# Optimization experiments

Measured on AMD Instinct MI355X. Metric: run time of the kernel, lower is better.

Reference implementation:

```python
import jax, jax.numpy as jnp
import numpy as np

D_MODEL = 1024
NUM_HEADS = 16


def setup_inputs() -> dict:
    key = jax.random.key(0)
    ks = jax.random.split(key, 11)
    B, T, D = 4, 2048, D_MODEL
    scale = 1.0 / np.sqrt(D)
    inp = {
        'q': jax.random.normal(ks[0], (B, T, D), jnp.float32),
        'k': jax.random.normal(ks[1], (B, T, D), jnp.float32),
        'v': jax.random.normal(ks[2], (B, T, D), jnp.float32),
        'W_q': jax.random.normal(ks[3], (D, D), jnp.float32) * scale,
        'b_q': jnp.zeros((D,), jnp.float32),
        'W_k': jax.random.normal(ks[4], (D, D), jnp.float32) * scale,
        'b_k': jnp.zeros((D,), jnp.float32),
        'W_v': jax.random.normal(ks[5], (D, D), jnp.float32) * scale,
        'b_v': jnp.zeros((D,), jnp.float32),
        'W_o': jax.random.normal(ks[6], (D, D), jnp.float32) * scale,
        'b_o': jnp.zeros((D,), jnp.float32),
    }
    return inp


def reference(q, k, v, W_q, b_q, W_k, b_k, W_v, b_v, W_o, b_o):
    B, T, D = q.shape
    H = NUM_HEADS
    hd = D // H  # head dim

    def split_heads(x):  # [B,T,D] -> [B,H,T,hd]
        return x.reshape(B, T, H, hd).transpose(0, 2, 1, 3)

    qh = split_heads(q @ W_q + b_q)
    kh = split_heads(k @ W_k + b_k)
    vh = split_heads(v @ W_v + b_v)

    score = jnp.einsum('bhqd,bhkd->bhqk', qh, kh) / jnp.sqrt(jnp.float32(hd))
    attn = jax.nn.softmax(score, axis=-1)
    out = jnp.einsum('bhqk,bhkd->bhqd', attn, vh)  # [B,H,T,hd]
    out = out.transpose(0, 2, 1, 3).reshape(B, T, D)
    return out @ W_o + b_o
```

## Files before the change

kernel.cpp:

```cpp
#include <hip/hip_runtime.h>

typedef __attribute__((ext_vector_type(8))) short s8v;
typedef __attribute__((ext_vector_type(4))) float f4v;
typedef __attribute__((ext_vector_type(16))) float f16v;
typedef __attribute__((ext_vector_type(8))) unsigned short u8v;
typedef __attribute__((ext_vector_type(4))) unsigned short u16x4;
typedef __attribute__((ext_vector_type(4))) unsigned int uint4v;

#define B_ 4
#define T_ 2048
#define D_ 1024
#define H_ 16
#define HD_ 64

__device__ __forceinline__ unsigned short f2bf(float f) {
  unsigned int u = __builtin_bit_cast(unsigned int, f);
  u += 0x7fffu + ((u >> 16) & 1u);
  return (unsigned short)(u >> 16);
}

__device__ __forceinline__ unsigned int packbf2(float lo, float hi) {
  unsigned int u0 = __builtin_bit_cast(unsigned int, lo) + 0x8000u;
  unsigned int u1 = __builtin_bit_cast(unsigned int, hi) + 0x8000u;
  return __builtin_amdgcn_perm(u1, u0, 0x07060302u);
}

__device__ __forceinline__ void gload_lds16(const void* g, void* l) {
  __builtin_amdgcn_global_load_lds(
      (const __attribute__((address_space(1))) unsigned int*)g,
      (__attribute__((address_space(3))) unsigned int*)l, 16, 0, 0);
}

__global__ __launch_bounds__(256) void cvt_bf16(const float* __restrict__ x,
                                                unsigned short* __restrict__ y) {
  size_t i = ((size_t)blockIdx.x * 256 + threadIdx.x) * 8;
  float4 a = *(const float4*)(x + i);
  float4 b = *(const float4*)(x + i + 4);
  u8v o;
  o[0] = f2bf(a.x); o[1] = f2bf(a.y); o[2] = f2bf(a.z); o[3] = f2bf(a.w);
  o[4] = f2bf(b.x); o[5] = f2bf(b.y); o[6] = f2bf(b.z); o[7] = f2bf(b.w);
  *(u8v*)(y + i) = o;
}

__global__ __launch_bounds__(256) void wt_cvt(
    const float* __restrict__ Wq, const float* __restrict__ Wk,
    const float* __restrict__ Wv, const float* __restrict__ Wo,
    unsigned short* __restrict__ Tq, unsigned short* __restrict__ Tk,
    unsigned short* __restrict__ Tv, unsigned short* __restrict__ To) {
  __shared__ unsigned short tile[32][33];
  int z = blockIdx.z;
  const float* W = (z == 0) ? Wq : (z == 1) ? Wk : (z == 2) ? Wv : Wo;
  unsigned short* Wt = (z == 0) ? Tq : (z == 1) ? Tk : (z == 2) ? Tv : To;
  int k0 = blockIdx.x * 32, n0 = blockIdx.y * 32;
  int t = threadIdx.x;
  int r = t >> 3, c = (t & 7) * 4;
  float4 v = *(const float4*)(W + (size_t)(k0 + r) * D_ + n0 + c);
  tile[r][c + 0] = f2bf(v.x);
  tile[r][c + 1] = f2bf(v.y);
  tile[r][c + 2] = f2bf(v.z);
  tile[r][c + 3] = f2bf(v.w);
  __syncthreads();
  u16x4 o;
  o[0] = tile[c + 0][r];
  o[1] = tile[c + 1][r];
  o[2] = tile[c + 2][r];
  o[3] = tile[c + 3][r];
  *(u16x4*)(Wt + (size_t)(n0 + r) * D_ + k0 + c) = o;
}

__global__ __launch_bounds__(256) void vt_tr(const unsigned short* __restrict__ Vp,
                                             unsigned short* __restrict__ Vt) {
  __shared__ unsigned short tile[32][36];
  int bh = blockIdx.z;
  int b = bh >> 4, h = bh & 15;
  int t0 = blockIdx.x * 32, d0 = blockIdx.y * 32;
  int r = threadIdx.x >> 3, c = (threadIdx.x & 7) * 4;
  u16x4 v = *(const u16x4*)(Vp + ((size_t)(b * T_ + t0 + r)) * D_ + h * HD_ + d0 + c);
  tile[r][c + 0] = v[0];
  tile[r][c + 1] = v[1];
  tile[r][c + 2] = v[2];
  tile[r][c + 3] = v[3];
  __syncthreads();
  u16x4 o;
  o[0] = tile[c + 0][r];
  o[1] = tile[c + 1][r];
  o[2] = tile[c + 2][r];
  o[3] = tile[c + 3][r];
  *(u16x4*)(Vt + ((size_t)bh * HD_ + d0 + r) * T_ + t0 + c) = o;
}

__global__ __launch_bounds__(256) void gemm_bf16(
    const unsigned short* __restrict__ A, const unsigned short* __restrict__ Bt,
    const float* __restrict__ bias, float* __restrict__ Cf,
    unsigned short* __restrict__ Cb, int M, int N, int K) {
  __shared__ unsigned short As[128 * 32];
  __shared__ unsigned short Bs[128 * 32];
  int tid = threadIdx.x;
  int wave = tid >> 6, lane = tid & 63;
  int dl = lane & 15, quad = lane >> 4;
  int wm = (wave >> 1) * 64, wn = (wave & 1) * 64;
  size_t m0 = (size_t)blockIdx.y * 128, n0 = (size_t)blockIdx.x * 128;
  f4v acc[4][4] = {};
  int g0 = wave * 128 + lane;
  int g1 = g0 + 64;
  const unsigned short* Ag0 = A + (m0 + (g0 >> 2)) * K + (g0 & 3) * 8;
  const unsigned short* Ag1 = A + (m0 + (g1 >> 2)) * K + (g1 & 3) * 8;
  const unsigned short* Bg0 = Bt + (n0 + (g0 >> 2)) * K + (g0 & 3) * 8;
  const unsigned short* Bg1 = Bt + (n0 + (g1 >> 2)) * K + (g1 & 3) * 8;
  unsigned short* la0 = &As[g0 * 8];
  unsigned short* la1 = &As[g1 * 8];
  unsigned short* lb0 = &Bs[g0 * 8];
  unsigned short* lb1 = &Bs[g1 * 8];

  for (int k0 = 0; k0 < K; k0 += 32) {
    gload_lds16(Ag0 + k0, la0);
    gload_lds16(Ag1 + k0, la1);
    gload_lds16(Bg0 + k0, lb0);
    gload_lds16(Bg1 + k0, lb1);
    __syncthreads();
    s8v af[4], bf4[4];
#pragma unroll
    for (int i = 0; i < 4; i++) af[i] = *(const s8v*)&As[(wm + i * 16 + dl) * 32 + quad * 8];
#pragma unroll
    for (int i = 0; i < 4; i++) bf4[i] = *(const s8v*)&Bs[(wn + i * 16 + dl) * 32 + quad * 8];
#pragma unroll
    for (int mi = 0; mi < 4; mi++)
#pragma unroll
      for (int ni = 0; ni < 4; ni++)
        acc[mi][ni] = __builtin_amdgcn_mfma_f32_16x16x32_bf16(af[mi], bf4[ni], acc[mi][ni], 0, 0, 0);
    __syncthreads();
  }

#pragma unroll
  for (int ni = 0; ni < 4; ni++) {
    size_t col = n0 + wn + ni * 16 + dl;
    float bv = bias[col];
#pragma unroll
    for (int mi = 0; mi < 4; mi++) {
#pragma unroll
      for (int r = 0; r < 4; r++) {
        size_t row = m0 + wm + mi * 16 + quad * 4 + r;
        float v = acc[mi][ni][r] + bv;
        if (Cb) Cb[row * N + col] = f2bf(v);
        else Cf[row * N + col] = v;
      }
    }
  }
}

__global__ __launch_bounds__(256) void attn(
    const unsigned short* __restrict__ Q, const unsigned short* __restrict__ K,
    const unsigned short* __restrict__ Vt, unsigned short* __restrict__ Ctx) {
  int tid = threadIdx.x;
  int wave = tid >> 6, lane = tid & 63;
  int l31 = lane & 31, hh = lane >> 5;
  int b = blockIdx.z, h = blockIdx.y;
  int qbase = blockIdx.x * 128 + wave * 32;
  const unsigned short* Qb = Q + ((size_t)(b * T_ + qbase + l31)) * D_ + h * HD_;
  const unsigned short* Kb = K + ((size_t)b * T_) * D_ + h * HD_;
  const unsigned short* Vb = Vt + ((size_t)(b * H_ + h)) * HD_ * T_;

  s8v qf[4];
#pragma unroll
  for (int ks = 0; ks < 4; ks++) qf[ks] = *(const s8v*)(Qb + ks * 16 + 8 * hh);

  f16v zero = {};
  f16v oacc[2] = {zero, zero};
  float l = 0.f;
  const float sc = 0.18033688011112042f;

  s8v kf[2][2][4];
#pragma unroll
  for (int ms = 0; ms < 2; ms++) {
    const unsigned short* kr = Kb + ((size_t)(ms * 32 + l31)) * D_;
#pragma unroll
    for (int ks = 0; ks < 4; ks++) kf[0][ms][ks] = *(const s8v*)(kr + ks * 16 + 8 * hh);
  }

#pragma unroll 2
  for (int it = 0; it < T_ / 64; ++it) {
    int kt = it * 64;
    int cur = it & 1, nxt = cur ^ 1;
    s8v vf[2][4];
#pragma unroll
    for (int md = 0; md < 2; md++) {
      const unsigned short* vr = Vb + ((size_t)(md * 32 + l31)) * T_ + kt;
#pragma unroll
      for (int kk = 0; kk < 4; kk++) vf[md][kk] = *(const s8v*)(vr + kk * 16 + 8 * hh);
    }
    int ktn = (kt + 64) & (T_ - 1);
#pragma unroll
    for (int ms = 0; ms < 2; ms++) {
      const unsigned short* kr = Kb + ((size_t)(ktn + ms * 32 + l31)) * D_;
#pragma unroll
      for (int ks = 0; ks < 4; ks++) kf[nxt][ms][ks] = *(const s8v*)(kr + ks * 16 + 8 * hh);
    }

    f16v sacc[2] = {zero, zero};
#pragma unroll
    for (int ks = 0; ks < 4; ks++)
#pragma unroll
      for (int ms = 0; ms < 2; ms++)
        sacc[ms] = __builtin_amdgcn_mfma_f32_32x32x16_bf16(kf[cur][ms][ks], qf[ks], sacc[ms], 0, 0, 0);

    unsigned int pk[2][8];
#pragma unroll
    for (int ms = 0; ms < 2; ms++)
#pragma unroll
      for (int i = 0; i < 8; i++) {
        float p0 = exp2f(__builtin_fmaf(sacc[ms][2 * i], sc, -16.f));
        float p1 = exp2f(__builtin_fmaf(sacc[ms][2 * i + 1], sc, -16.f));
        l += p0 + p1;
        pk[ms][i] = packbf2(p0, p1);
      }

#pragma unroll
    for (int kk = 0; kk < 4; kk++) {
      int ms = kk >> 1, e4 = (kk & 1) * 4;
      unsigned int y0 = __shfl_xor(pk[ms][e4 + 2], 32);
      unsigned int y1 = __shfl_xor(pk[ms][e4 + 3], 32);
      unsigned int y2 = __shfl_xor(pk[ms][e4 + 0], 32);
      unsigned int y3 = __shfl_xor(pk[ms][e4 + 1], 32);
      uint4v pd;
      pd[0] = hh ? y0 : pk[ms][e4 + 0];
      pd[1] = hh ? y1 : pk[ms][e4 + 1];
      pd[2] = hh ? pk[ms][e4 + 2] : y2;
      pd[3] = hh ? pk[ms][e4 + 3] : y3;
      s8v pf = __builtin_bit_cast(s8v, pd);
#pragma unroll
      for (int md = 0; md < 2; md++)
        oacc[md] = __builtin_amdgcn_mfma_f32_32x32x16_bf16(vf[md][kk], pf, oacc[md], 0, 0, 0);
    }
  }

  l += __shfl_xor(l, 32);
  float inv = 1.0f / l;
  unsigned short* crow = Ctx + ((size_t)(b * T_ + qbase + l31)) * D_ + h * HD_;
#pragma unroll
  for (int md = 0; md < 2; md++)
#pragma unroll
    for (int hi = 0; hi < 4; hi++) {
      unsigned int w0 = (unsigned int)f2bf(oacc[md][hi * 4 + 0] * inv) |
                        ((unsigned int)f2bf(oacc[md][hi * 4 + 1] * inv) << 16);
      unsigned int w1 = (unsigned int)f2bf(oacc[md][hi * 4 + 2] * inv) |
                        ((unsigned int)f2bf(oacc[md][hi * 4 + 3] * inv) << 16);
      unsigned int* dst = (unsigned int*)(crow + md * 32 + hi * 8 + 4 * hh);
      dst[0] = w0;
      dst[1] = w1;
    }
}

extern "C" void kernel_launch(void* const* d_in, const int* in_sizes, int n_in,
                              void* d_out, int out_size, void* d_ws, size_t ws_size,
                              hipStream_t stream) {
  const float* q = (const float*)d_in[0];
  const float* k = (const float*)d_in[1];
  const float* v = (const float*)d_in[2];
  const float* Wq = (const float*)d_in[3];
  const float* bq = (const float*)d_in[4];
  const float* Wk = (const float*)d_in[5];
  const float* bk = (const float*)d_in[6];
  const float* Wv = (const float*)d_in[7];
  const float* bv = (const float*)d_in[8];
  const float* Wo = (const float*)d_in[9];
  const float* bo = (const float*)d_in[10];
  float* out = (float*)d_out;

  char* ws = (char*)d_ws;
  const size_t MB = 1ull << 20;
  unsigned short* xb = (unsigned short*)(ws + 0);
  unsigned short* Tq = (unsigned short*)(ws + 16 * MB);
  unsigned short* Tk = (unsigned short*)(ws + 18 * MB);
  unsigned short* Tv = (unsigned short*)(ws + 20 * MB);
  unsigned short* To = (unsigned short*)(ws + 22 * MB);
  unsigned short* Qp = (unsigned short*)(ws + 24 * MB);
  unsigned short* Kp = (unsigned short*)(ws + 40 * MB);
  unsigned short* Vp = (unsigned short*)(ws + 56 * MB);
  unsigned short* Vt = (unsigned short*)(ws + 72 * MB);
  const int M = B_ * T_;

  wt_cvt<<<dim3(32, 32, 4), 256, 0, stream>>>(Wq, Wk, Wv, Wo, Tq, Tk, Tv, To);

  cvt_bf16<<<dim3(4096), 256, 0, stream>>>(q, xb);
  gemm_bf16<<<dim3(D_ / 128, M / 128), 256, 0, stream>>>(xb, Tq, bq, nullptr, Qp, M, D_, D_);
  cvt_bf16<<<dim3(4096), 256, 0, stream>>>(k, xb);
  gemm_bf16<<<dim3(D_ / 128, M / 128), 256, 0, stream>>>(xb, Tk, bk, nullptr, Kp, M, D_, D_);
  cvt_bf16<<<dim3(4096), 256, 0, stream>>>(v, xb);
  gemm_bf16<<<dim3(D_ / 128, M / 128), 256, 0, stream>>>(xb, Tv, bv, nullptr, Vp, M, D_, D_);

  vt_tr<<<dim3(T_ / 32, HD_ / 32, B_ * H_), 256, 0, stream>>>(Vp, Vt);
  attn<<<dim3(T_ / 128, H_, B_), 256, 0, stream>>>(Qp, Kp, Vt, xb);
  gemm_bf16<<<dim3(D_ / 128, M / 128), 256, 0, stream>>>(xb, To, bo, out, nullptr, M, D_, D_);
}
```

Measured before the change: 584.5 us.

## Fuse fp32 conversion into batched QKV GEMM and repack K/V into MFMA fragment layout

Drops the separate fp32-to-bf16 conversion passes. The QKV GEMM now loads fp32 activations straight into LDS and converts them during fragment reads, and a single z-batched launch covers all three projections. LDS tiles get an XOR swizzle to reduce bank conflicts. K and V are repacked into a contiguous per-lane fragment layout so the attention kernel's loads are coalesced, replacing the strided K reads and the V transpose. The fp32 A tile doubles LDS traffic, and the repacks add extra passes over memory.

```diff
diff --git a/kernel.cpp b/kernel.cpp
--- a/kernel.cpp
+++ b/kernel.cpp
@@ -29,17 +29,6 @@
   __builtin_amdgcn_global_load_lds(
       (const __attribute__((address_space(1))) unsigned int*)g,
       (__attribute__((address_space(3))) unsigned int*)l, 16, 0, 0);
-}
-
-__global__ __launch_bounds__(256) void cvt_bf16(const float* __restrict__ x,
-                                                unsigned short* __restrict__ y) {
-  size_t i = ((size_t)blockIdx.x * 256 + threadIdx.x) * 8;
-  float4 a = *(const float4*)(x + i);
-  float4 b = *(const float4*)(x + i + 4);
-  u8v o;
-  o[0] = f2bf(a.x); o[1] = f2bf(a.y); o[2] = f2bf(a.z); o[3] = f2bf(a.w);
-  o[4] = f2bf(b.x); o[5] = f2bf(b.y); o[6] = f2bf(b.z); o[7] = f2bf(b.w);
-  *(u8v*)(y + i) = o;
 }
 
 __global__ __launch_bounds__(256) void wt_cvt(
@@ -68,61 +57,123 @@
   *(u16x4*)(Wt + (size_t)(n0 + r) * D_ + k0 + c) = o;
 }
 
-__global__ __launch_bounds__(256) void vt_tr(const unsigned short* __restrict__ Vp,
-                                             unsigned short* __restrict__ Vt) {
-  __shared__ unsigned short tile[32][36];
-  int bh = blockIdx.z;
-  int b = bh >> 4, h = bh & 15;
-  int t0 = blockIdx.x * 32, d0 = blockIdx.y * 32;
-  int r = threadIdx.x >> 3, c = (threadIdx.x & 7) * 4;
-  u16x4 v = *(const u16x4*)(Vp + ((size_t)(b * T_ + t0 + r)) * D_ + h * HD_ + d0 + c);
-  tile[r][c + 0] = v[0];
-  tile[r][c + 1] = v[1];
-  tile[r][c + 2] = v[2];
-  tile[r][c + 3] = v[3];
+__global__ __launch_bounds__(256) void repack_k(const unsigned short* __restrict__ Kp,
+                                                unsigned short* __restrict__ Kf) {
+  unsigned int g = blockIdx.x * 256 + threadIdx.x;
+  unsigned int bh = g >> 14;
+  unsigned int r = g & 16383;
+  unsigned int c32 = r >> 8;
+  unsigned int ks = (r >> 6) & 3;
+  unsigned int l2 = r & 63;
+  unsigned int l = l2 >> 1, hh = l2 & 1;
+  unsigned int b = bh >> 4, h = bh & 15;
+  size_t row = (size_t)b * T_ + c32 * 32 + l;
+  u8v v = *(const u8v*)(Kp + row * D_ + h * HD_ + ks * 16 + hh * 8);
+  *(u8v*)(Kf + (size_t)g * 8) = v;
+}
+
+__global__ __launch_bounds__(256) void repack_v(const unsigned short* __restrict__ Vp,
+                                                unsigned short* __restrict__ Vf) {
+  __shared__ unsigned short tl[64][72];
+  unsigned int c64 = blockIdx.x;
+  unsigned int bh = blockIdx.y;
+  unsigned int b = bh >> 4, h = bh & 15;
+  int tid = threadIdx.x;
+#pragma unroll
+  for (int i = 0; i < 2; i++) {
+    int s = i * 256 + tid;
+    int row = s >> 3, cir = s & 7;
+    u8v v = *(const u8v*)(Vp + ((size_t)(b * T_ + c64 * 64 + row)) * D_ + h * HD_ + cir * 8);
+    *(u8v*)&tl[row][cir * 8] = v;
+  }
   __syncthreads();
-  u16x4 o;
-  o[0] = tile[c + 0][r];
-  o[1] = tile[c + 1][r];
-  o[2] = tile[c + 2][r];
-  o[3] = tile[c + 3][r];
-  *(u16x4*)(Vt + ((size_t)bh * HD_ + d0 + r) * T_ + t0 + c) = o;
-}
-
-__global__ __launch_bounds__(256) void gemm_bf16(
-    const unsigned short* __restrict__ A, const unsigned short* __restrict__ Bt,
-    const float* __restrict__ bias, float* __restrict__ Cf,
-    unsigned short* __restrict__ Cb, int M, int N, int K) {
-  __shared__ unsigned short As[128 * 32];
-  __shared__ unsigned short Bs[128 * 32];
+#pragma unroll
+  for (int i = 0; i < 2; i++) {
+    int s = i * 256 + tid;
+    int mdkk = s >> 6;
+    int l2 = s & 63;
+    int l = l2 >> 1, hh = l2 & 1;
+    int md = mdkk >> 2, kk = mdkk & 3;
+    u8v o;
+#pragma unroll
+    for (int j = 0; j < 8; j++) o[j] = tl[kk * 16 + hh * 8 + j][md * 32 + l];
+    *(u8v*)(Vf + ((size_t)(bh * 32 + c64) * 8 + mdkk) * 512 + l2 * 8) = o;
+  }
+}
+
+struct GemmArgs {
+  const void* A[3];
+  const unsigned short* B[3];
+  const float* bias[3];
+  void* C[3];
+};
+
+template <bool AF32, bool OUTF32>
+__global__ __launch_bounds__(256) void gemm128(GemmArgs args, int M, int N, int K) {
+  __shared__ unsigned char smem[(AF32 ? 16384 : 8192) + 8192];
+  unsigned char* AsB = smem;
+  unsigned char* BsB = smem + (AF32 ? 16384 : 8192);
+  int z = blockIdx.z;
+  const float* Af = (const float*)args.A[z];
+  const unsigned short* Ab = (const unsigned short*)args.A[z];
+  const unsigned short* Bt = args.B[z];
+  const float* bias = args.bias[z];
   int tid = threadIdx.x;
   int wave = tid >> 6, lane = tid & 63;
   int dl = lane & 15, quad = lane >> 4;
   int wm = (wave >> 1) * 64, wn = (wave & 1) * 64;
   size_t m0 = (size_t)blockIdx.y * 128, n0 = (size_t)blockIdx.x * 128;
   f4v acc[4][4] = {};
-  int g0 = wave * 128 + lane;
-  int g1 = g0 + 64;
-  const unsigned short* Ag0 = A + (m0 + (g0 >> 2)) * K + (g0 & 3) * 8;
-  const unsigned short* Ag1 = A + (m0 + (g1 >> 2)) * K + (g1 & 3) * 8;
-  const unsigned short* Bg0 = Bt + (n0 + (g0 >> 2)) * K + (g0 & 3) * 8;
-  const unsigned short* Bg1 = Bt + (n0 + (g1 >> 2)) * K + (g1 & 3) * 8;
-  unsigned short* la0 = &As[g0 * 8];
-  unsigned short* la1 = &As[g1 * 8];
-  unsigned short* lb0 = &Bs[g0 * 8];
-  unsigned short* lb1 = &Bs[g1 * 8];
 
   for (int k0 = 0; k0 < K; k0 += 32) {
-    gload_lds16(Ag0 + k0, la0);
-    gload_lds16(Ag1 + k0, la1);
-    gload_lds16(Bg0 + k0, lb0);
-    gload_lds16(Bg1 + k0, lb1);
+    if constexpr (AF32) {
+#pragma unroll
+      for (int i = 0; i < 4; i++) {
+        int s = i * 256 + tid;
+        int row = s >> 3, cs = s & 7, csrc = cs ^ (row & 7);
+        gload_lds16(Af + (m0 + row) * K + k0 + csrc * 4, AsB + s * 16);
+      }
+    } else {
+#pragma unroll
+      for (int i = 0; i < 2; i++) {
+        int s = i * 256 + tid;
+        int row = s >> 2, cs = s & 3, csrc = cs ^ ((row >> 1) & 3);
+        gload_lds16(Ab + (m0 + row) * K + k0 + csrc * 8, AsB + s * 16);
+      }
+    }
+#pragma unroll
+    for (int i = 0; i < 2; i++) {
+      int s = i * 256 + tid;
+      int row = s >> 2, cs = s & 3, csrc = cs ^ ((row >> 1) & 3);
+      gload_lds16(Bt + (n0 + row) * K + k0 + csrc * 8, BsB + s * 16);
+    }
     __syncthreads();
     s8v af[4], bf4[4];
 #pragma unroll
-    for (int i = 0; i < 4; i++) af[i] = *(const s8v*)&As[(wm + i * 16 + dl) * 32 + quad * 8];
-#pragma unroll
-    for (int i = 0; i < 4; i++) bf4[i] = *(const s8v*)&Bs[(wn + i * 16 + dl) * 32 + quad * 8];
+    for (int i = 0; i < 4; i++) {
+      int row = wm + i * 16 + dl;
+      if constexpr (AF32) {
+        const float* Ar = (const float*)AsB + row * 32;
+        int f = row & 7;
+        float4 lo = *(const float4*)(Ar + ((2 * quad) ^ f) * 4);
+        float4 hi = *(const float4*)(Ar + ((2 * quad + 1) ^ f) * 4);
+        uint4v p;
+        p[0] = packbf2(lo.x, lo.y);
+        p[1] = packbf2(lo.z, lo.w);
+        p[2] = packbf2(hi.x, hi.y);
+        p[3] = packbf2(hi.z, hi.w);
+        af[i] = __builtin_bit_cast(s8v, p);
+      } else {
+        const unsigned short* Ar = (const unsigned short*)AsB + row * 32;
+        af[i] = *(const s8v*)(Ar + (quad ^ ((row >> 1) & 3)) * 8);
+      }
+    }
+#pragma unroll
+    for (int i = 0; i < 4; i++) {
+      int row = wn + i * 16 + dl;
+      const unsigned short* Br = (const unsigned short*)BsB + row * 32;
+      bf4[i] = *(const s8v*)(Br + (quad ^ ((row >> 1) & 3)) * 8);
+    }
 #pragma unroll
     for (int mi = 0; mi < 4; mi++)
 #pragma unroll
@@ -141,24 +192,26 @@
       for (int r = 0; r < 4; r++) {
         size_t row = m0 + wm + mi * 16 + quad * 4 + r;
         float v = acc[mi][ni][r] + bv;
-        if (Cb) Cb[row * N + col] = f2bf(v);
-        else Cf[row * N + col] = v;
+        if constexpr (OUTF32) ((float*)args.C[z])[row * N + col] = v;
+        else ((unsigned short*)args.C[z])[row * N + col] = f2bf(v);
       }
     }
   }
 }
 
 __global__ __launch_bounds__(256) void attn(
-    const unsigned short* __restrict__ Q, const unsigned short* __restrict__ K,
-    const unsigned short* __restrict__ Vt, unsigned short* __restrict__ Ctx) {
+    const unsigned short* __restrict__ Q, const unsigned short* __restrict__ Kf,
+    const unsigned short* __restrict__ Vf, unsigned short* __restrict__ Ctx) {
   int tid = threadIdx.x;
   int wave = tid >> 6, lane = tid & 63;
   int l31 = lane & 31, hh = lane >> 5;
   int b = blockIdx.z, h = blockIdx.y;
+  int bh = b * H_ + h;
   int qbase = blockIdx.x * 128 + wave * 32;
   const unsigned short* Qb = Q + ((size_t)(b * T_ + qbase + l31)) * D_ + h * HD_;
-  const unsigned short* Kb = K + ((size_t)b * T_) * D_ + h * HD_;
-  const unsigned short* Vb = Vt + ((size_t)(b * H_ + h)) * HD_ * T_;
+  const unsigned short* Kfb = Kf + (size_t)bh * (T_ * HD_);
+  const unsigned short* Vfb = Vf + (size_t)bh * (T_ * HD_);
+  int lc = (l31 * 2 + hh) * 8;
 
   s8v qf[4];
 #pragma unroll
@@ -171,11 +224,10 @@
 
   s8v kf[2][2][4];
 #pragma unroll
-  for (int ms = 0; ms < 2; ms++) {
-    const unsigned short* kr = Kb + ((size_t)(ms * 32 + l31)) * D_;
-#pragma unroll
-    for (int ks = 0; ks < 4; ks++) kf[0][ms][ks] = *(const s8v*)(kr + ks * 16 + 8 * hh);
-  }
+  for (int ms = 0; ms < 2; ms++)
+#pragma unroll
+    for (int ks = 0; ks < 4; ks++)
+      kf[0][ms][ks] = *(const s8v*)(Kfb + (size_t)(ms * 4 + ks) * 512 + lc);
 
 #pragma unroll 2
   for (int it = 0; it < T_ / 64; ++it) {
@@ -183,18 +235,16 @@
     int cur = it & 1, nxt = cur ^ 1;
     s8v vf[2][4];
 #pragma unroll
-    for (int md = 0; md < 2; md++) {
-      const unsigned short* vr = Vb + ((size_t)(md * 32 + l31)) * T_ + kt;
-#pragma unroll
-      for (int kk = 0; kk < 4; kk++) vf[md][kk] = *(const s8v*)(vr + kk * 16 + 8 * hh);
-    }
+    for (int md = 0; md < 2; md++)
+#pragma unroll
+      for (int kk = 0; kk < 4; kk++)
+        vf[md][kk] = *(const s8v*)(Vfb + ((size_t)(kt >> 6) * 8 + md * 4 + kk) * 512 + lc);
     int ktn = (kt + 64) & (T_ - 1);
 #pragma unroll
-    for (int ms = 0; ms < 2; ms++) {
-      const unsigned short* kr = Kb + ((size_t)(ktn + ms * 32 + l31)) * D_;
-#pragma unroll
-      for (int ks = 0; ks < 4; ks++) kf[nxt][ms][ks] = *(const s8v*)(kr + ks * 16 + 8 * hh);
-    }
+    for (int ms = 0; ms < 2; ms++)
+#pragma unroll
+      for (int ks = 0; ks < 4; ks++)
+        kf[nxt][ms][ks] = *(const s8v*)(Kfb + ((size_t)((ktn >> 5) + ms) * 4 + ks) * 512 + lc);
 
     f16v sacc[2] = {zero, zero};
 #pragma unroll
@@ -240,10 +290,8 @@
   for (int md = 0; md < 2; md++)
 #pragma unroll
     for (int hi = 0; hi < 4; hi++) {
-      unsigned int w0 = (unsigned int)f2bf(oacc[md][hi * 4 + 0] * inv) |
-                        ((unsigned int)f2bf(oacc[md][hi * 4 + 1] * inv) << 16);
-      unsigned int w1 = (unsigned int)f2bf(oacc[md][hi * 4 + 2] * inv) |
-                        ((unsigned int)f2bf(oacc[md][hi * 4 + 3] * inv) << 16);
+      unsigned int w0 = packbf2(oacc[md][hi * 4 + 0] * inv, oacc[md][hi * 4 + 1] * inv);
+      unsigned int w1 = packbf2(oacc[md][hi * 4 + 2] * inv, oacc[md][hi * 4 + 3] * inv);
       unsigned int* dst = (unsigned int*)(crow + md * 32 + hi * 8 + 4 * hh);
       dst[0] = w0;
       dst[1] = w1;
@@ -268,27 +316,33 @@
 
   char* ws = (char*)d_ws;
   const size_t MB = 1ull << 20;
-  unsigned short* xb = (unsigned short*)(ws + 0);
-  unsigned short* Tq = (unsigned short*)(ws + 16 * MB);
-  unsigned short* Tk = (unsigned short*)(ws + 18 * MB);
-  unsigned short* Tv = (unsigned short*)(ws + 20 * MB);
-  unsigned short* To = (unsigned short*)(ws + 22 * MB);
-  unsigned short* Qp = (unsigned short*)(ws + 24 * MB);
-  unsigned short* Kp = (unsigned short*)(ws + 40 * MB);
-  unsigned short* Vp = (unsigned short*)(ws + 56 * MB);
-  unsigned short* Vt = (unsigned short*)(ws + 72 * MB);
+  unsigned short* Tq = (unsigned short*)(ws + 0 * MB);
+  unsigned short* Tk = (unsigned short*)(ws + 2 * MB);
+  unsigned short* Tv = (unsigned short*)(ws + 4 * MB);
+  unsigned short* To = (unsigned short*)(ws + 6 * MB);
+  unsigned short* Qp = (unsigned short*)(ws + 8 * MB);
+  unsigned short* Kp = (unsigned short*)(ws + 24 * MB);
+  unsigned short* Vp = (unsigned short*)(ws + 40 * MB);
+  unsigned short* Kf = (unsigned short*)(ws + 56 * MB);
+  unsigned short* Vf = (unsigned short*)(ws + 72 * MB);
+  unsigned short* Ctx = Kp;
   const int M = B_ * T_;
 
   wt_cvt<<<dim3(32, 32, 4), 256, 0, stream>>>(Wq, Wk, Wv, Wo, Tq, Tk, Tv, To);
 
-  cvt_bf16<<<dim3(4096), 256, 0, stream>>>(q, xb);
-  gemm_bf16<<<dim3(D_ / 128, M / 128), 256, 0, stream>>>(xb, Tq, bq, nullptr, Qp, M, D_, D_);
-  cvt_bf16<<<dim3(4096), 256, 0, stream>>>(k, xb);
-  gemm_bf16<<<dim3(D_ / 128, M / 128), 256, 0, stream>>>(xb, Tk, bk, nullptr, Kp, M, D_, D_);
-  cvt_bf16<<<dim3(4096), 256, 0, stream>>>(v, xb);
-  gemm_bf16<<<dim3(D_ / 128, M / 128), 256, 0, stream>>>(xb, Tv, bv, nullptr, Vp, M, D_, D_);
-
-  vt_tr<<<dim3(T_ / 32, HD_ / 32, B_ * H_), 256, 0, stream>>>(Vp, Vt);
-  attn<<<dim3(T_ / 128, H_, B_), 256, 0, stream>>>(Qp, Kp, Vt, xb);
-  gemm_bf16<<<dim3(D_ / 128, M / 128), 256, 0, stream>>>(xb, To, bo, out, nullptr, M, D_, D_);
-}
+  GemmArgs ga;
+  ga.A[0] = q;  ga.A[1] = k;  ga.A[2] = v;
+  ga.B[0] = Tq; ga.B[1] = Tk; ga.B[2] = Tv;
+  ga.bias[0] = bq; ga.bias[1] = bk; ga.bias[2] = bv;
+  ga.C[0] = Qp; ga.C[1] = Kp; ga.C[2] = Vp;
+  gemm128<true, false><<<dim3(D_ / 128, M / 128, 3), 256, 0, stream>>>(ga, M, D_, D_);
+
+  repack_k<<<dim3(4096), 256, 0, stream>>>(Kp, Kf);
+  repack_v<<<dim3(32, 64), 256, 0, stream>>>(Vp, Vf);
+
+  attn<<<dim3(T_ / 128, H_, B_), 256, 0, stream>>>(Qp, Kf, Vf, Ctx);
+
+  GemmArgs go;
+  go.A[0] = Ctx; go.B[0] = To; go.bias[0] = bo; go.C[0] = out;
+  gemm128<false, true><<<dim3(D_ / 128, M / 128, 1), 256, 0, stream>>>(go, M, D_, D_);
+}
```

Result: faster. 515.4 us (-11.8%).
